# Optimization experiments

Measured on AMD Instinct MI355X. Metric: run time of the kernel, lower is better.

Reference implementation:

```python
import jax, jax.numpy as jnp
import numpy as np

N_NODES = 100000
N_EDGES = 3200000
D_IN = 256
D_HID = 256
N_CLASS = 40


def setup_inputs() -> dict:
    key = jax.random.key(0)
    ks = jax.random.split(key, 8)
    x = jax.random.normal(ks[0], (N_NODES, D_IN), dtype=jnp.float32)
    edge_index = jax.random.randint(ks[1], (2, N_EDGES), 0, N_NODES, dtype=jnp.int64)
    s1 = 1.0 / np.sqrt(D_IN)
    s2 = 1.0 / np.sqrt(D_HID)
    W1_l = jax.random.normal(ks[2], (D_IN, D_HID), dtype=jnp.float32) * s1
    W1_r = jax.random.normal(ks[3], (D_IN, D_HID), dtype=jnp.float32) * s1
    b1 = jnp.zeros((D_HID,), dtype=jnp.float32)
    W2_l = jax.random.normal(ks[4], (D_HID, N_CLASS), dtype=jnp.float32) * s2
    W2_r = jax.random.normal(ks[5], (D_HID, N_CLASS), dtype=jnp.float32) * s2
    b2 = jnp.zeros((N_CLASS,), dtype=jnp.float32)
    return {"x": x, "edge_index": edge_index, "W1_l": W1_l, "W1_r": W1_r,
            "b1": b1, "W2_l": W2_l, "W2_r": W2_r, "b2": b2}


def _sage_conv(h, src, dst, deg_inv, Wl, Wr, b):
    # mean-aggregate source features into targets, then linear transforms
    agg = jax.ops.segment_sum(h[src], dst, num_segments=N_NODES)  # [N, d]
    agg = agg * deg_inv[:, None]
    return agg @ Wl + h @ Wr + b


def reference(x, edge_index, W1_l, W1_r, b1, W2_l, W2_r, b2):
    src, dst = edge_index[0], edge_index[1]
    deg = jax.ops.segment_sum(jnp.ones((src.shape[0],), dtype=x.dtype), dst,
                              num_segments=N_NODES)
    deg_inv = 1.0 / jnp.maximum(deg, 1.0)
    h = jax.nn.relu(_sage_conv(x, src, dst, deg_inv, W1_l, W1_r, b1))
    out = _sage_conv(h, src, dst, deg_inv, W2_l, W2_r, b2)
    return jax.nn.log_softmax(out, axis=1)
```

## Files before the change

kernel.cpp:

```cpp
#include <hip/hip_runtime.h>
#include <hip/hip_bf16.h>

#define THREADS 256
#define NB_MAX 400
#define NPH 13

typedef __attribute__((ext_vector_type(8))) short bf16x8;
typedef __attribute__((ext_vector_type(4))) float f32x4;
typedef __attribute__((ext_vector_type(2))) float f32x2;

__device__ __forceinline__ unsigned short f2b(float f) {
    __hip_bfloat16 h = __float2bfloat16(f);
    return *reinterpret_cast<unsigned short*>(&h);
}
__device__ __forceinline__ unsigned char f2q(float v) {
    int q = __builtin_amdgcn_cvt_pk_fp8_f32(v, v, 0, false);
    return (unsigned char)(q & 0xff);
}
__device__ __forceinline__ void gload_lds16(const void* g, void* l) {
    __builtin_amdgcn_global_load_lds(
        (const __attribute__((address_space(1))) void*)g,
        (__attribute__((address_space(3))) void*)l, 16, 0, 0);
}

__global__ __launch_bounds__(256) void k_hist_cvt(
    const int* __restrict__ dst, int E, int nbk, int* __restrict__ gcnt, int nsb,
    const float* __restrict__ x, unsigned short* __restrict__ xb, unsigned char* __restrict__ xq,
    int N, int Npad,
    const float* __restrict__ W1l, const float* __restrict__ W1r,
    const float* __restrict__ W2l, const float* __restrict__ W2r,
    unsigned short* __restrict__ WbT, unsigned short* __restrict__ WbT2) {
    __shared__ int lc[NB_MAX];
    const int tid = threadIdx.x;
    if ((int)blockIdx.x < nsb) {
        for (int i = tid; i < nbk; i += 256) lc[i] = 0;
        __syncthreads();
        const int stride = nsb * 256;
        for (int e = blockIdx.x * 256 + tid; e < E; e += stride)
            atomicAdd(&lc[dst[e] >> 8], 1);
        __syncthreads();
        for (int i = tid; i < nbk; i += 256)
            if (lc[i]) atomicAdd(&gcnt[i], lc[i]);
        return;
    }
    int i = ((int)blockIdx.x - nsb) * 256 + tid;
    const int nxu = Npad * 32;
    if (i < nxu) {
        int row = i >> 5;
        unsigned short o[8];
        int q0 = 0, q1 = 0;
        if (row < N) {
            float4 v0 = reinterpret_cast<const float4*>(x)[2 * (size_t)i];
            float4 v1 = reinterpret_cast<const float4*>(x)[2 * (size_t)i + 1];
            o[0] = f2b(v0.x); o[1] = f2b(v0.y); o[2] = f2b(v0.z); o[3] = f2b(v0.w);
            o[4] = f2b(v1.x); o[5] = f2b(v1.y); o[6] = f2b(v1.z); o[7] = f2b(v1.w);
            q0 = __builtin_amdgcn_cvt_pk_fp8_f32(v0.x, v0.y, q0, false);
            q0 = __builtin_amdgcn_cvt_pk_fp8_f32(v0.z, v0.w, q0, true);
            q1 = __builtin_amdgcn_cvt_pk_fp8_f32(v1.x, v1.y, q1, false);
            q1 = __builtin_amdgcn_cvt_pk_fp8_f32(v1.z, v1.w, q1, true);
        } else {
            #pragma unroll
            for (int j = 0; j < 8; ++j) o[j] = 0;
        }
        reinterpret_cast<uint4*>(xb)[i] = *reinterpret_cast<uint4*>(o);
        reinterpret_cast<uint2*>(xq)[i] = make_uint2((unsigned)q0, (unsigned)q1);
        return;
    }
    int idx = i - nxu;
    if (idx < 131072) {
        int n = idx >> 9, k = idx & 511;
        float v = (k < 256) ? W1l[(size_t)k * 256 + n] : W1r[(size_t)(k - 256) * 256 + n];
        WbT[idx] = f2b(v);
    } else if (idx < 131072 + 20480) {
        int j = idx - 131072;
        int n = j >> 8, k = j & 255;
        float v = (n < 40) ? W2l[(size_t)k * 40 + n] : W2r[(size_t)k * 40 + (n - 40)];
        WbT2[j] = f2b(v);
    }
}

__global__ __launch_bounds__(512) void k_scanb(const int* __restrict__ gcnt, int* __restrict__ bptr,
                                               int* __restrict__ gcur, int nbk, int E) {
    __shared__ int sm[512];
    const int t = threadIdx.x;
    int v = (t < nbk) ? gcnt[t] : 0;
    sm[t] = v; __syncthreads();
    for (int off = 1; off < 512; off <<= 1) {
        int u = (t >= off) ? sm[t - off] : 0; __syncthreads();
        sm[t] += u; __syncthreads();
    }
    if (t < nbk) {
        int ex = sm[t] - v;
        bptr[t] = ex;
        gcur[t] = ex;
    }
    if (t == 0) bptr[nbk] = E;
}

__global__ __launch_bounds__(256) void k_bucket_scatter(const int* __restrict__ src, const int* __restrict__ dst,
                                                        int* __restrict__ gcur, unsigned* __restrict__ pairs,
                                                        int E, int nbk) {
    __shared__ int cnt[NB_MAX];
    __shared__ int base[NB_MAX];
    const int tid = threadIdx.x;
    const int e0 = blockIdx.x * 8192;
    for (int i = tid; i < nbk; i += 256) cnt[i] = 0;
    __syncthreads();
    #pragma unroll
    for (int j = 0; j < 32; ++j) {
        int e = e0 + j * 256 + tid;
        if (e < E) atomicAdd(&cnt[dst[e] >> 8], 1);
    }
    __syncthreads();
    for (int i = tid; i < nbk; i += 256)
        base[i] = cnt[i] ? atomicAdd(&gcur[i], cnt[i]) : 0;
    __syncthreads();
    #pragma unroll
    for (int j = 0; j < 32; ++j) {
        int e = e0 + j * 256 + tid;
        if (e < E) {
            int d = dst[e];
            int p = atomicAdd(&base[d >> 8], 1);
            pairs[p] = ((unsigned)src[e] << 8) | ((unsigned)d & 255u);
        }
    }
}

__global__ __launch_bounds__(256) void k_bucket_csr(const int* __restrict__ bptr, const unsigned* __restrict__ pairs,
                                                    int* __restrict__ rowptr, float* __restrict__ dinv,
                                                    int* __restrict__ csr_src, int N, int nbk, int E) {
    __shared__ int pc[256 * NPH];
    __shared__ int sm[256];
    __shared__ int nodebase[256];
    const int b = blockIdx.x;
    const int tid = threadIdx.x;
    const int e0 = bptr[b], e1 = bptr[b + 1];

    #pragma unroll
    for (int i = 0; i < NPH; ++i) pc[i * 256 + tid] = 0;
    __syncthreads();
    for (int e = e0 + tid; e < e1; e += 256) {
        unsigned u = pairs[e];
        int n = (int)(u & 255u);
        int ph = (int)(u >> 8) >> 13;
        atomicAdd(&pc[ph * 256 + n], 1);
    }
    __syncthreads();
    int run = 0;
    #pragma unroll
    for (int ph = 0; ph < NPH; ++ph) {
        int c = pc[ph * 256 + tid];
        pc[ph * 256 + tid] = run;
        run += c;
    }
    int d = run;
    sm[tid] = d; __syncthreads();
    for (int off = 1; off < 256; off <<= 1) {
        int u = (tid >= off) ? sm[tid - off] : 0; __syncthreads();
        sm[tid] += u; __syncthreads();
    }
    int ex = sm[tid] - d;
    int node = (b << 8) + tid;
    int nb_ = e0 + ex;
    nodebase[tid] = nb_;
    if (node < N) {
        rowptr[node] = nb_;
        dinv[node] = 1.0f / (float)max(d, 1);
    }
    if (b == nbk - 1 && tid == 0) rowptr[N] = E;
    __syncthreads();
    #pragma unroll
    for (int ph = 0; ph < NPH; ++ph) pc[ph * 256 + tid] += nodebase[tid];
    __syncthreads();
    for (int e = e0 + tid; e < e1; e += 256) {
        unsigned u = pairs[e];
        int n = (int)(u & 255u);
        int s = (int)(u >> 8);
        int p = atomicAdd(&pc[(s >> 13) * 256 + n], 1);
        csr_src[p] = s;
    }
}

__global__ __launch_bounds__(256) void k_agg1(const int* __restrict__ rowptr, const int* __restrict__ csr_src,
                                              const float* __restrict__ dinv, const unsigned char* __restrict__ xq,
                                              unsigned short* __restrict__ aggb, int N, int Npad) {
    int gid = blockIdx.x * THREADS + threadIdx.x;
    int node = gid >> 5, lane = gid & 31;
    if (node >= N) {
        if (node < Npad)
            reinterpret_cast<uint4*>(aggb + (size_t)node * 256 + lane * 8)[0] = make_uint4(0, 0, 0, 0);
        return;
    }
    const int e0 = rowptr[node], e1 = rowptr[node + 1];
    const unsigned char* xl = xq + (size_t)lane * 8;
    f32x2 acc[4];
    #pragma unroll
    for (int j = 0; j < 4; ++j) acc[j] = (f32x2){0.f, 0.f};
    for (int eb = e0; eb < e1; eb += 32) {
        int n = min(32, e1 - eb);
        int sidx = (eb + lane < e1) ? csr_src[eb + lane] : 0;
        int j = 0;
        for (; j + 7 < n; j += 8) {
            uint2 vv[8];
            #pragma unroll
            for (int q = 0; q < 8; ++q) {
                int s = __shfl(sidx, j + q, 32);
                vv[q] = *reinterpret_cast<const uint2*>(xl + (size_t)s * 256);
            }
            #pragma unroll
            for (int q = 0; q < 8; ++q) {
                acc[0] += __builtin_amdgcn_cvt_pk_f32_fp8((int)vv[q].x, false);
                acc[1] += __builtin_amdgcn_cvt_pk_f32_fp8((int)vv[q].x, true);
                acc[2] += __builtin_amdgcn_cvt_pk_f32_fp8((int)vv[q].y, false);
                acc[3] += __builtin_amdgcn_cvt_pk_f32_fp8((int)vv[q].y, true);
            }
        }
        for (; j < n; ++j) {
            int s = __shfl(sidx, j, 32);
            uint2 v = *reinterpret_cast<const uint2*>(xl + (size_t)s * 256);
            acc[0] += __builtin_amdgcn_cvt_pk_f32_fp8((int)v.x, false);
            acc[1] += __builtin_amdgcn_cvt_pk_f32_fp8((int)v.x, true);
            acc[2] += __builtin_amdgcn_cvt_pk_f32_fp8((int)v.y, false);
            acc[3] += __builtin_amdgcn_cvt_pk_f32_fp8((int)v.y, true);
        }
    }
    const float ds = dinv[node];
    unsigned short o[8];
    #pragma unroll
    for (int j = 0; j < 4; ++j) {
        o[2 * j + 0] = f2b(acc[j].x * ds);
        o[2 * j + 1] = f2b(acc[j].y * ds);
    }
    *reinterpret_cast<uint4*>(aggb + (size_t)node * 256 + lane * 8) = *reinterpret_cast<uint4*>(o);
}

__global__ __launch_bounds__(512) void k_gemm1(
    const unsigned short* __restrict__ aggb, const unsigned short* __restrict__ xb,
    const unsigned short* __restrict__ WbT, const float* __restrict__ b1,
    unsigned short* __restrict__ hb, int M)
{
    __shared__ unsigned short As[128 * 64];
    __shared__ unsigned short Bs[256 * 64];

    const int tid  = threadIdx.x;
    const int lane = tid & 63;
    const int wave = tid >> 6;
    const int row0 = blockIdx.x * 128;
    const int wm0  = (wave >> 2) * 64;
    const int wn0  = (wave & 3) * 64;

    const int ldr = lane >> 3;
    const int lsw = ((lane & 7) ^ ldr) * 8;

    f32x4 acc[4][4];
    #pragma unroll
    for (int m = 0; m < 4; ++m)
        #pragma unroll
        for (int n = 0; n < 4; ++n)
            acc[m][n] = (f32x4){0.f, 0.f, 0.f, 0.f};

    for (int kt = 0; kt < 8; ++kt) {
        const unsigned short* Abase = (kt < 4) ? aggb : xb;
        const int kcol = (kt & 3) * 64;
        __syncthreads();
        #pragma unroll
        for (int i = 0; i < 2; ++i) {
            const int c = wave * 2 + i;
            const unsigned short* ga = Abase + (size_t)(row0 + c * 8 + ldr) * 256 + kcol + lsw;
            gload_lds16(ga, &As[c * 512]);
        }
        #pragma unroll
        for (int i = 0; i < 4; ++i) {
            const int c = wave * 4 + i;
            const unsigned short* gb = WbT + (size_t)(c * 8 + ldr) * 512 + kt * 64 + lsw;
            gload_lds16(gb, &Bs[c * 512]);
        }
        __syncthreads();
        #pragma unroll
        for (int kk = 0; kk < 2; ++kk) {
            bf16x8 af[4], bf[4];
            #pragma unroll
            for (int m = 0; m < 4; ++m) {
                const int r = wm0 + m * 16 + (lane & 15);
                const int s = (kk * 4 + (lane >> 4)) ^ (r & 7);
                af[m] = *reinterpret_cast<const bf16x8*>(&As[r * 64 + s * 8]);
            }
            #pragma unroll
            for (int n = 0; n < 4; ++n) {
                const int r = wn0 + n * 16 + (lane & 15);
                const int s = (kk * 4 + (lane >> 4)) ^ (r & 7);
                bf[n] = *reinterpret_cast<const bf16x8*>(&Bs[r * 64 + s * 8]);
            }
            #pragma unroll
            for (int m = 0; m < 4; ++m)
                #pragma unroll
                for (int n = 0; n < 4; ++n)
                    acc[m][n] = __builtin_amdgcn_mfma_f32_16x16x32_bf16(af[m], bf[n], acc[m][n], 0, 0, 0);
        }
    }

    const int crow = (lane >> 4) * 4;
    const int ccol = lane & 15;
    #pragma unroll
    for (int n = 0; n < 4; ++n) {
        const int col = wn0 + n * 16 + ccol;
        const float bias = b1[col];
        #pragma unroll
        for (int m = 0; m < 4; ++m) {
            const int rbase = row0 + wm0 + m * 16 + crow;
            #pragma unroll
            for (int r = 0; r < 4; ++r) {
                const int row = rbase + r;
                if (row < M) {
                    float v = fmaxf(acc[m][n][r] + bias, 0.f);
                    hb[(size_t)row * 256 + col] = f2b(v);
                }
            }
        }
    }
}

__global__ __launch_bounds__(256) void k_gemm2(
    const unsigned short* __restrict__ hb, const unsigned short* __restrict__ WbT2,
    const float* __restrict__ b2,
    unsigned char* __restrict__ Tq, float* __restrict__ Up, int M)
{
    __shared__ unsigned short As[128 * 64];
    __shared__ unsigned short Bs2[80 * 264];

    const int tid  = threadIdx.x;
    const int lane = tid & 63;
    const int wave = tid >> 6;
    const int row0 = blockIdx.x * 128;

    const int ldr = lane >> 3;
    const int lsw = ((lane & 7) ^ ldr) * 8;

    for (int idx = tid; idx < 80 * 32; idx += 256) {
        int row = idx >> 5, un = idx & 31;
        uint4 d = *reinterpret_cast<const uint4*>(WbT2 + (size_t)row * 256 + un * 8);
        *reinterpret_cast<uint4*>(&Bs2[row * 264 + un * 8]) = d;
    }

    f32x4 acc[2][5];
    #pragma unroll
    for (int m = 0; m < 2; ++m)
        #pragma unroll
        for (int n = 0; n < 5; ++n)
            acc[m][n] = (f32x4){0.f, 0.f, 0.f, 0.f};

    for (int kt = 0; kt < 4; ++kt) {
        __syncthreads();
        #pragma unroll
        for (int i = 0; i < 4; ++i) {
            const int c = wave * 4 + i;
            const unsigned short* ga = hb + (size_t)(row0 + c * 8 + ldr) * 256 + kt * 64 + lsw;
            gload_lds16(ga, &As[c * 512]);
        }
        __syncthreads();
        #pragma unroll
        for (int kk = 0; kk < 2; ++kk) {
            bf16x8 af[2], bf[5];
            #pragma unroll
            for (int m = 0; m < 2; ++m) {
                const int r = wave * 32 + m * 16 + (lane & 15);
                const int s = (kk * 4 + (lane >> 4)) ^ (r & 7);
                af[m] = *reinterpret_cast<const bf16x8*>(&As[(r & 127) * 64 + s * 8]);
            }
            #pragma unroll
            for (int n = 0; n < 5; ++n) {
                const int r = n * 16 + (lane & 15);
                bf[n] = *reinterpret_cast<const bf16x8*>(&Bs2[r * 264 + kt * 64 + kk * 32 + (lane >> 4) * 8]);
            }
            #pragma unroll
            for (int m = 0; m < 2; ++m)
                #pragma unroll
                for (int n = 0; n < 5; ++n)
                    acc[m][n] = __builtin_amdgcn_mfma_f32_16x16x32_bf16(af[m], bf[n], acc[m][n], 0, 0, 0);
        }
    }

    const int crow = (lane >> 4) * 4;
    const int ccol = lane & 15;
    #pragma unroll
    for (int n = 0; n < 5; ++n) {
        const int col = n * 16 + ccol;
        #pragma unroll
        for (int m = 0; m < 2; ++m) {
            const int rbase = row0 + wave * 32 + m * 16 + crow;
            #pragma unroll
            for (int r = 0; r < 4; ++r) {
                const int row = rbase + r;
                if (row < M) {
                    float v = acc[m][n][r];
                    if (col < 40)
                        Tq[(size_t)row * 64 + col] = f2q(v);
                    else
                        Up[(size_t)row * 40 + (col - 40)] = v + b2[col - 40];
                }
            }
        }
    }
    for (int i = tid; i < 128 * 24; i += 256) {
        int r = i / 24, c = 40 + (i % 24);
        int row = row0 + r;
        if (row < M) Tq[(size_t)row * 64 + c] = 0;
    }
}

__global__ __launch_bounds__(256) void k_final(const int* __restrict__ rowptr, const int* __restrict__ csr_src,
                                               const float* __restrict__ dinv, const unsigned char* __restrict__ Tq,
                                               const float* __restrict__ Up, float* __restrict__ out, int N) {
    int gid = blockIdx.x * THREADS + threadIdx.x;
    int node = gid >> 6, lane = gid & 63;
    if (node >= N) return;
    const int e0 = rowptr[node], e1 = rowptr[node + 1];
    const int c8 = lane & 7;
    const int e5 = lane >> 3;
    f32x2 acc[4];
    #pragma unroll
    for (int i = 0; i < 4; ++i) acc[i] = (f32x2){0.f, 0.f};
    for (int eb = e0; eb < e1; eb += 64) {
        int sidx = (eb + lane < e1) ? csr_src[eb + lane] : 0;
        int nn = min(64, e1 - eb);
        for (int jb = 0; jb < nn; jb += 8) {
            int ei = jb + e5;
            int s = __shfl(sidx, ei & 63, 64);
            if (ei < nn) {
                uint2 u = *reinterpret_cast<const uint2*>(Tq + (size_t)s * 64 + c8 * 8);
                acc[0] += __builtin_amdgcn_cvt_pk_f32_fp8((int)u.x, false);
                acc[1] += __builtin_amdgcn_cvt_pk_f32_fp8((int)u.x, true);
                acc[2] += __builtin_amdgcn_cvt_pk_f32_fp8((int)u.y, false);
                acc[3] += __builtin_amdgcn_cvt_pk_f32_fp8((int)u.y, true);
            }
        }
    }
    #pragma unroll
    for (int st = 8; st <= 32; st <<= 1) {
        #pragma unroll
        for (int i = 0; i < 4; ++i) {
            acc[i].x += __shfl_xor(acc[i].x, st, 64);
            acc[i].y += __shfl_xor(acc[i].y, st, 64);
        }
    }
    const bool act = (e5 == 0) && (c8 < 5);
    float v[8];
    float m = -1e30f;
    if (act) {
        const float ds = dinv[node];
        float4 ua = *reinterpret_cast<const float4*>(Up + (size_t)node * 40 + c8 * 8);
        float4 ub = *reinterpret_cast<const float4*>(Up + (size_t)node * 40 + c8 * 8 + 4);
        v[0] = acc[0].x * ds + ua.x; v[1] = acc[0].y * ds + ua.y;
        v[2] = acc[1].x * ds + ua.z; v[3] = acc[1].y * ds + ua.w;
        v[4] = acc[2].x * ds + ub.x; v[5] = acc[2].y * ds + ub.y;
        v[6] = acc[3].x * ds + ub.z; v[7] = acc[3].y * ds + ub.w;
        #pragma unroll
        for (int i = 0; i < 8; ++i) m = fmaxf(m, v[i]);
    }
    #pragma unroll
    for (int o = 4; o > 0; o >>= 1) m = fmaxf(m, __shfl_xor(m, o, 8));
    float e = 0.f;
    if (act) {
        #pragma unroll
        for (int i = 0; i < 8; ++i) e += expf(v[i] - m);
    }
    #pragma unroll
    for (int o = 4; o > 0; o >>= 1) e += __shfl_xor(e, o, 8);
    float ls = logf(e);
    if (act) {
        float4 oa, ob;
        oa.x = v[0] - m - ls; oa.y = v[1] - m - ls; oa.z = v[2] - m - ls; oa.w = v[3] - m - ls;
        ob.x = v[4] - m - ls; ob.y = v[5] - m - ls; ob.z = v[6] - m - ls; ob.w = v[7] - m - ls;
        *reinterpret_cast<float4*>(out + (size_t)node * 40 + c8 * 8) = oa;
        *reinterpret_cast<float4*>(out + (size_t)node * 40 + c8 * 8 + 4) = ob;
    }
}

extern "C" void kernel_launch(void* const* d_in, const int* in_sizes, int n_in,
                              void* d_out, int out_size, void* d_ws, size_t ws_size,
                              hipStream_t stream) {
    const float* x   = (const float*)d_in[0];
    const int*   ei  = (const int*)d_in[1];
    const float* W1l = (const float*)d_in[2];
    const float* W1r = (const float*)d_in[3];
    const float* b1  = (const float*)d_in[4];
    const float* W2l = (const float*)d_in[5];
    const float* W2r = (const float*)d_in[6];
    const float* b2  = (const float*)d_in[7];
    float* out = (float*)d_out;

    const int N = in_sizes[0] / 256;
    const int E = in_sizes[1] / 2;
    const int Npad = ((N + 127) / 128) * 128;
    const int nbk = (N + 255) / 256;
    const int* src = ei;
    const int* dst = ei + E;

    char* ws = (char*)d_ws;
    size_t off = 0;
    int*   gcnt    = (int*)(ws + off); off += (size_t)NB_MAX * 4;
    int*   bptr    = (int*)(ws + off); off += (size_t)(NB_MAX + 1) * 4;
    int*   gcur    = (int*)(ws + off); off += (size_t)NB_MAX * 4;
    int*   rowptr  = (int*)(ws + off); off += (size_t)(N + 1) * 4;
    float* dinv    = (float*)(ws + off); off += (size_t)N * 4;
    off = (off + 255) & ~(size_t)255;
    unsigned* pairs = (unsigned*)(ws + off); off += (size_t)E * 4;
    int*   csr_src = (int*)(ws + off); off += (size_t)E * 4;
    off = (off + 255) & ~(size_t)255;
    unsigned short* xb   = (unsigned short*)(ws + off); off += (size_t)Npad * 256 * 2;
    unsigned char*  xq   = (unsigned char*)(ws + off);  off += (size_t)Npad * 256;
    unsigned short* aggb = (unsigned short*)(ws + off); off += (size_t)Npad * 256 * 2;
    unsigned short* hb   = (unsigned short*)(ws + off); off += (size_t)Npad * 256 * 2;
    unsigned short* WbT  = (unsigned short*)(ws + off); off += (size_t)256 * 512 * 2;
    unsigned short* WbT2 = (unsigned short*)(ws + off); off += (size_t)80 * 256 * 2;
    off = (off + 255) & ~(size_t)255;
    unsigned char*  Tq   = (unsigned char*)(ws + off);  off += (size_t)Npad * 64;
    off = (off + 255) & ~(size_t)255;
    float*          Up   = (float*)(ws + off);          off += (size_t)Npad * 40 * 4;

    hipMemsetAsync(gcnt, 0, (size_t)NB_MAX * 4, stream);

    const int nsb = (E + 8191) / 8192;
    const int ncvt_blocks = (Npad * 32 + 131072 + 20480 + THREADS - 1) / THREADS;
    k_hist_cvt<<<nsb + ncvt_blocks, THREADS, 0, stream>>>(dst, E, nbk, gcnt, nsb,
                                                          x, xb, xq, N, Npad,
                                                          W1l, W1r, W2l, W2r, WbT, WbT2);
    k_scanb<<<1, 512, 0, stream>>>(gcnt, bptr, gcur, nbk, E);
    k_bucket_scatter<<<nsb, THREADS, 0, stream>>>(src, dst, gcur, pairs, E, nbk);
    k_bucket_csr<<<nbk, THREADS, 0, stream>>>(bptr, pairs, rowptr, dinv, csr_src, N, nbk, E);

    k_agg1<<<((size_t)Npad * 32 + THREADS - 1) / THREADS, THREADS, 0, stream>>>(rowptr, csr_src, dinv, xq, aggb, N, Npad);

    k_gemm1<<<Npad / 128, 512, 0, stream>>>(aggb, xb, WbT, b1, hb, N);

    k_gemm2<<<Npad / 128, THREADS, 0, stream>>>(hb, WbT2, b2, Tq, Up, N);

    k_final<<<((size_t)N * 64 + THREADS - 1) / THREADS, THREADS, 0, stream>>>(rowptr, csr_src, dinv, Tq, Up, out, N);
}
```

Before: 399.8 us.

## Drop source-phase bucketing in CSR build and memset Tq padding once

Result: no change. 405.3 us (+1.4%).

```diff
diff --git a/kernel.cpp b/kernel.cpp
--- a/kernel.cpp
+++ b/kernel.cpp
@@ -3,7 +3,6 @@
 
 #define THREADS 256
 #define NB_MAX 400
-#define NPH 13
 
 typedef __attribute__((ext_vector_type(8))) short bf16x8;
 typedef __attribute__((ext_vector_type(4))) float f32x4;
@@ -129,31 +128,19 @@
 __global__ __launch_bounds__(256) void k_bucket_csr(const int* __restrict__ bptr, const unsigned* __restrict__ pairs,
                                                     int* __restrict__ rowptr, float* __restrict__ dinv,
                                                     int* __restrict__ csr_src, int N, int nbk, int E) {
-    __shared__ int pc[256 * NPH];
+    __shared__ int deg[256];
     __shared__ int sm[256];
-    __shared__ int nodebase[256];
+    __shared__ int cur[256];
     const int b = blockIdx.x;
     const int tid = threadIdx.x;
     const int e0 = bptr[b], e1 = bptr[b + 1];
 
-    #pragma unroll
-    for (int i = 0; i < NPH; ++i) pc[i * 256 + tid] = 0;
+    deg[tid] = 0;
     __syncthreads();
-    for (int e = e0 + tid; e < e1; e += 256) {
-        unsigned u = pairs[e];
-        int n = (int)(u & 255u);
-        int ph = (int)(u >> 8) >> 13;
-        atomicAdd(&pc[ph * 256 + n], 1);
-    }
+    for (int e = e0 + tid; e < e1; e += 256)
+        atomicAdd(&deg[pairs[e] & 255u], 1);
     __syncthreads();
-    int run = 0;
-    #pragma unroll
-    for (int ph = 0; ph < NPH; ++ph) {
-        int c = pc[ph * 256 + tid];
-        pc[ph * 256 + tid] = run;
-        run += c;
-    }
-    int d = run;
+    int d = deg[tid];
     sm[tid] = d; __syncthreads();
     for (int off = 1; off < 256; off <<= 1) {
         int u = (tid >= off) ? sm[tid - off] : 0; __syncthreads();
@@ -161,23 +148,17 @@
     }
     int ex = sm[tid] - d;
     int node = (b << 8) + tid;
-    int nb_ = e0 + ex;
-    nodebase[tid] = nb_;
+    cur[tid] = e0 + ex;
     if (node < N) {
-        rowptr[node] = nb_;
+        rowptr[node] = e0 + ex;
         dinv[node] = 1.0f / (float)max(d, 1);
     }
     if (b == nbk - 1 && tid == 0) rowptr[N] = E;
-    __syncthreads();
-    #pragma unroll
-    for (int ph = 0; ph < NPH; ++ph) pc[ph * 256 + tid] += nodebase[tid];
     __syncthreads();
     for (int e = e0 + tid; e < e1; e += 256) {
         unsigned u = pairs[e];
-        int n = (int)(u & 255u);
-        int s = (int)(u >> 8);
-        int p = atomicAdd(&pc[(s >> 13) * 256 + n], 1);
-        csr_src[p] = s;
+        int p = atomicAdd(&cur[u & 255u], 1);
+        csr_src[p] = (int)(u >> 8);
     }
 }
 
@@ -400,11 +381,6 @@
                 }
             }
         }
-    }
-    for (int i = tid; i < 128 * 24; i += 256) {
-        int r = i / 24, c = 40 + (i % 24);
-        int row = row0 + r;
-        if (row < M) Tq[(size_t)row * 64 + c] = 0;
     }
 }
 
@@ -519,6 +495,7 @@
     float*          Up   = (float*)(ws + off);          off += (size_t)Npad * 40 * 4;
 
     hipMemsetAsync(gcnt, 0, (size_t)NB_MAX * 4, stream);
+    hipMemsetAsync(Tq, 0, (size_t)Npad * 64, stream);
 
     const int nsb = (E + 8191) / 8192;
     const int ncvt_blocks = (Npad * 32 + 131072 + 20480 + THREADS - 1) / THREADS;
```
